# Kernel optimization log

Measured on AMD Instinct MI355X. Metric: run time of the kernel, lower is better.

The kernel has to match this reference:

```python
import jax, jax.numpy as jnp
import numpy as np

N_NODES = 100000
N_EDGES = 1600000
F_IN = 64
F_OUT = 64


def setup_inputs() -> dict:
    key = jax.random.key(0)
    k1, k2, k3 = jax.random.split(key, 3)
    x = jax.random.normal(k1, (1, 1, N_NODES, F_IN), dtype=jnp.float32)
    edge_index = jax.random.randint(k2, (2, N_EDGES), 0, N_NODES, dtype=jnp.int32)
    # xavier-init linear weight [F_IN, F_OUT], zero bias (xavier_zero_bias)
    scale = jnp.sqrt(2.0 / (F_IN + F_OUT)).astype(jnp.float32)
    weight = jax.random.normal(k3, (F_IN, F_OUT), dtype=jnp.float32) * scale
    bias = jnp.zeros((F_OUT,), dtype=jnp.float32)
    return {"x": x, "edge_index": edge_index, "weight": weight, "bias": bias}


def reference(x, edge_index, weight, bias):
    # x: [B, T, N, F_in]
    B, T, N, _ = x.shape
    # linear transform
    h = jnp.einsum('btnf,fo->btno', x, weight) + bias  # [B,T,N,F_out]
    # add self loops
    loops = jnp.arange(N, dtype=edge_index.dtype)
    src = jnp.concatenate([edge_index[0], loops])  # [E+N]
    dst = jnp.concatenate([edge_index[1], loops])  # [E+N]
    w = jnp.ones(src.shape[0], dtype=h.dtype)
    # symmetric GCN normalization: D^{-1/2} A D^{-1/2} (degree over dst)
    deg = jnp.zeros((N,), dtype=h.dtype).at[dst].add(w)
    inv_sqrt = jnp.clip(deg, 1e-9) ** -0.5
    norm = inv_sqrt[dst] * w * inv_sqrt[src]  # [E+N]
    # gather src features, scale by norm, scatter-add to dst
    msg = h[:, :, src, :] * norm[None, None, :, None]  # [B,T,E+N,F_out]
    out = jnp.zeros_like(h).at[:, :, dst, :].add(msg)  # [B,T,N,F_out]
    # GraphConvBase post: activation (gelu), dropout=0, norm=identity
    return jax.nn.gelu(out)
```

## Files before the change

### kernel.cpp

```cpp
#include <hip/hip_runtime.h>
#include <hip/hip_fp16.h>
#include <math.h>

#define N_NODES 100000
#define N_EDGES 1600000
#define F_DIM 64
#define BSH 9
#define BNODES 512
#define NBUCK ((N_NODES + BNODES - 1) / BNODES)
#define CAP 16384
#define EPT 8
#define TILE (256 * EPT)

__global__ __launch_bounds__(256) void init_k(int* __restrict__ bcur) {
    int i = blockIdx.x * 256 + threadIdx.x;
    if (i < NBUCK) bcur[i] = i * CAP;
}

__global__ __launch_bounds__(256) void pass1_k(const int* __restrict__ src,
                                               const int* __restrict__ dst,
                                               int* __restrict__ bcur,
                                               unsigned int* __restrict__ tmp, int E) {
    __shared__ int lcnt[NBUCK];
    __shared__ int lbase[NBUCK];
    for (int i = threadIdx.x; i < NBUCK; i += 256) lcnt[i] = 0;
    __syncthreads();

    int4 sreg[EPT / 4], dreg[EPT / 4];
    int base4 = blockIdx.x * (TILE / 4);
#pragma unroll
    for (int j = 0; j < EPT / 4; ++j) {
        int i4 = base4 + j * 256 + threadIdx.x;
        if (i4 < E / 4) {
            sreg[j] = ((const int4*)src)[i4];
            dreg[j] = ((const int4*)dst)[i4];
            atomicAdd(&lcnt[dreg[j].x >> BSH], 1);
            atomicAdd(&lcnt[dreg[j].y >> BSH], 1);
            atomicAdd(&lcnt[dreg[j].z >> BSH], 1);
            atomicAdd(&lcnt[dreg[j].w >> BSH], 1);
        } else {
            dreg[j].x = -1;
        }
    }
    __syncthreads();
    for (int b = threadIdx.x; b < NBUCK; b += 256) {
        int c = lcnt[b];
        lbase[b] = c ? atomicAdd(&bcur[b], c) : 0;
        lcnt[b] = 0;
    }
    __syncthreads();
#pragma unroll
    for (int j = 0; j < EPT / 4; ++j) {
        if (dreg[j].x >= 0) {
            int d, s, b, r;
            d = dreg[j].x; s = sreg[j].x; b = d >> BSH;
            r = atomicAdd(&lcnt[b], 1);
            tmp[lbase[b] + r] = (unsigned int)s | ((unsigned int)(d & (BNODES - 1)) << 17);
            d = dreg[j].y; s = sreg[j].y; b = d >> BSH;
            r = atomicAdd(&lcnt[b], 1);
            tmp[lbase[b] + r] = (unsigned int)s | ((unsigned int)(d & (BNODES - 1)) << 17);
            d = dreg[j].z; s = sreg[j].z; b = d >> BSH;
            r = atomicAdd(&lcnt[b], 1);
            tmp[lbase[b] + r] = (unsigned int)s | ((unsigned int)(d & (BNODES - 1)) << 17);
            d = dreg[j].w; s = sreg[j].w; b = d >> BSH;
            r = atomicAdd(&lcnt[b], 1);
            tmp[lbase[b] + r] = (unsigned int)s | ((unsigned int)(d & (BNODES - 1)) << 17);
        }
    }
}

__global__ __launch_bounds__(512) void passB_k(unsigned int* __restrict__ tmp,
                                               const int* __restrict__ bcur,
                                               unsigned int* __restrict__ rowinfo,
                                               float* __restrict__ inv) {
    __shared__ unsigned int buf[CAP];
    __shared__ int cnt[BNODES];
    __shared__ int cur[BNODES];
    __shared__ int ls[BNODES];
    int b = blockIdx.x;
    int beg0 = b * CAP;
    int cntb = bcur[b] - beg0;
    int tid = threadIdx.x;

    cnt[tid] = 0;
    __syncthreads();
    for (int i = tid; i < cntb; i += 512) {
        unsigned int v = tmp[beg0 + i];
        buf[i] = v;
        atomicAdd(&cnt[v >> 17], 1);
    }
    __syncthreads();

    int a = cnt[tid];
    ls[tid] = a;
    __syncthreads();
    for (int off = 1; off < BNODES; off <<= 1) {
        int p = (tid >= off) ? ls[tid - off] : 0;
        __syncthreads();
        ls[tid] += p;
        __syncthreads();
    }
    int p0 = beg0 + ls[tid] - a;
    cur[tid] = p0;
    int n = (b << BSH) + tid;
    if (n < N_NODES) {
        rowinfo[n] = (unsigned int)p0 | ((unsigned int)a << 22);
        inv[n] = rsqrtf((float)(a + 1));
    }
    __syncthreads();

    for (int i = tid; i < cntb; i += 512) {
        unsigned int v = buf[i];
        int pos = atomicAdd(&cur[v >> 17], 1);
        tmp[pos] = v & 0x1FFFFu;
    }
}

__global__ __launch_bounds__(128) void linear_k(const float* __restrict__ x,
                                                const float* __restrict__ W,
                                                const float* __restrict__ bias,
                                                const float* __restrict__ inv,
                                                __half* __restrict__ h, int N) {
    __shared__ float Ws[F_DIM][F_DIM];
    __shared__ float bs[F_DIM];
    for (int i = threadIdx.x; i < F_DIM * F_DIM; i += 128) Ws[i >> 6][i & 63] = W[i];
    if (threadIdx.x < F_DIM) bs[threadIdx.x] = bias[threadIdx.x];
    __syncthreads();

    int n = blockIdx.x * 128 + threadIdx.x;
    if (n >= N) return;

    float xr[F_DIM];
    const float4* xp = (const float4*)(x + (size_t)n * F_DIM);
#pragma unroll
    for (int k4 = 0; k4 < 16; ++k4) {
        float4 v = xp[k4];
        xr[k4 * 4 + 0] = v.x; xr[k4 * 4 + 1] = v.y;
        xr[k4 * 4 + 2] = v.z; xr[k4 * 4 + 3] = v.w;
    }
    float invn = inv[n];
    __half* hp = h + (size_t)n * F_DIM;
#pragma unroll 1
    for (int f0 = 0; f0 < F_DIM; f0 += 4) {
        float a0 = bs[f0 + 0], a1 = bs[f0 + 1], a2 = bs[f0 + 2], a3 = bs[f0 + 3];
#pragma unroll
        for (int k = 0; k < F_DIM; ++k) {
            float xv = xr[k];
            a0 += xv * Ws[k][f0 + 0];
            a1 += xv * Ws[k][f0 + 1];
            a2 += xv * Ws[k][f0 + 2];
            a3 += xv * Ws[k][f0 + 3];
        }
        union { __half2 h2[2]; float2 f2; } u;
        u.h2[0] = __floats2half2_rn(a0 * invn, a1 * invn);
        u.h2[1] = __floats2half2_rn(a2 * invn, a3 * invn);
        *((float2*)(hp + f0)) = u.f2;
    }
}

__device__ __forceinline__ float gelu1(float x) {
    float x3 = x * x * x;
    float t = tanhf(0.7978845608028654f * (x + 0.044715f * x3));
    return 0.5f * x * (1.0f + t);
}

__global__ __launch_bounds__(256) void gather_k(const __half* __restrict__ h,
                                                const float* __restrict__ inv,
                                                const unsigned int* __restrict__ rowinfo,
                                                const unsigned int* __restrict__ esrc,
                                                float* __restrict__ out, int N) {
    int n = blockIdx.x * 4 + (threadIdx.x >> 6);
    if (n >= N) return;
    int lane = threadIdx.x & 63;
    int eslot = lane >> 4;
    int fq = lane & 15;

    unsigned int ri = rowinfo[n];
    int beg = (int)(ri & 0x3FFFFFu);
    int deg = (int)(ri >> 22);

    __half2 acc0 = __floats2half2_rn(0.f, 0.f);
    __half2 acc1 = acc0;
    int k = eslot;
    for (; k + 12 < deg; k += 16) {
        int s0 = (int)esrc[beg + k];
        int s1 = (int)esrc[beg + k + 4];
        int s2 = (int)esrc[beg + k + 8];
        int s3 = (int)esrc[beg + k + 12];
        union { float2 f; __half2 h2[2]; } u0, u1, u2, u3;
        u0.f = *((const float2*)(h + (size_t)s0 * F_DIM) + fq);
        u1.f = *((const float2*)(h + (size_t)s1 * F_DIM) + fq);
        u2.f = *((const float2*)(h + (size_t)s2 * F_DIM) + fq);
        u3.f = *((const float2*)(h + (size_t)s3 * F_DIM) + fq);
        acc0 = __hadd2(acc0, __hadd2(__hadd2(u0.h2[0], u1.h2[0]), __hadd2(u2.h2[0], u3.h2[0])));
        acc1 = __hadd2(acc1, __hadd2(__hadd2(u0.h2[1], u1.h2[1]), __hadd2(u2.h2[1], u3.h2[1])));
    }
    for (; k < deg; k += 4) {
        int s0 = (int)esrc[beg + k];
        union { float2 f; __half2 h2[2]; } u0;
        u0.f = *((const float2*)(h + (size_t)s0 * F_DIM) + fq);
        acc0 = __hadd2(acc0, u0.h2[0]);
        acc1 = __hadd2(acc1, u0.h2[1]);
    }
    float2 a = __half22float2(acc0);
    float2 b2 = __half22float2(acc1);
    float ax = a.x, ay = a.y, az = b2.x, aw = b2.y;
    ax += __shfl_xor(ax, 16); ay += __shfl_xor(ay, 16);
    az += __shfl_xor(az, 16); aw += __shfl_xor(aw, 16);
    ax += __shfl_xor(ax, 32); ay += __shfl_xor(ay, 32);
    az += __shfl_xor(az, 32); aw += __shfl_xor(aw, 32);

    if (eslot == 0) {
        float invn = inv[n];
        union { float2 f; __half2 h2[2]; } us;
        us.f = *((const float2*)(h + (size_t)n * F_DIM) + fq);
        float2 s0 = __half22float2(us.h2[0]);
        float2 s1 = __half22float2(us.h2[1]);
        float4 o;
        o.x = gelu1((ax + s0.x) * invn);
        o.y = gelu1((ay + s0.y) * invn);
        o.z = gelu1((az + s1.x) * invn);
        o.w = gelu1((aw + s1.y) * invn);
        ((float4*)(out + (size_t)n * F_DIM))[fq] = o;
    }
}

extern "C" void kernel_launch(void* const* d_in, const int* in_sizes, int n_in,
                              void* d_out, int out_size, void* d_ws, size_t ws_size,
                              hipStream_t stream) {
    const float* x    = (const float*)d_in[0];
    const int*   ei   = (const int*)d_in[1];
    const float* W    = (const float*)d_in[2];
    const float* bias = (const float*)d_in[3];
    float* out = (float*)d_out;

    const int* src = ei;
    const int* dst = ei + N_EDGES;

    unsigned int* tmp     = (unsigned int*)d_ws;
    unsigned int* rowinfo = tmp + (size_t)NBUCK * CAP;
    float*        inv     = (float*)(rowinfo + N_NODES);
    int*          bcur    = (int*)(inv + N_NODES);
    size_t off = (size_t)(bcur + NBUCK) - (size_t)d_ws;
    off = (off + 31) & ~(size_t)31;
    __half* h = (__half*)((char*)d_ws + off);

    init_k<<<(NBUCK + 255) / 256, 256, 0, stream>>>(bcur);
    pass1_k<<<(N_EDGES + TILE - 1) / TILE, 256, 0, stream>>>(src, dst, bcur, tmp, N_EDGES);
    passB_k<<<NBUCK, 512, 0, stream>>>(tmp, bcur, rowinfo, inv);
    linear_k<<<(N_NODES + 127) / 128, 128, 0, stream>>>(x, W, bias, inv, h, N_NODES);
    gather_k<<<(N_NODES + 3) / 4, 256, 0, stream>>>(h, inv, rowinfo, tmp, out, N_NODES);
}
```

Measured before the change: 131.1 us.

## Fuse edge bucketing with linear transform and move source normalization into gather

Edge bucketing and the dense linear transform now run in one launch, with blocks split by index, so the two independent phases overlap. Because the linear stage no longer needs per-node degrees, the source-side inverse-sqrt scaling moves into the gather, which reads inv[src] per edge and accumulates in fp32 FMAs instead of fp16 adds. passB drops its shared staging buffer, writes into a separate esrc array with 1024 threads, and bucket counters are zeroed by a memset instead of an init kernel. EPT and CAP change as well. The cost is an extra random inv load per edge and more ALU work in the gather. CAP=12288 also leaves less headroom against bucket overflow.

```diff
diff --git a/kernel.cpp b/kernel.cpp
--- a/kernel.cpp
+++ b/kernel.cpp
@@ -8,153 +8,149 @@
 #define BSH 9
 #define BNODES 512
 #define NBUCK ((N_NODES + BNODES - 1) / BNODES)
-#define CAP 16384
-#define EPT 8
+#define CAP 12288
+#define EPT 32
 #define TILE (256 * EPT)
-
-__global__ __launch_bounds__(256) void init_k(int* __restrict__ bcur) {
-    int i = blockIdx.x * 256 + threadIdx.x;
-    if (i < NBUCK) bcur[i] = i * CAP;
-}
-
-__global__ __launch_bounds__(256) void pass1_k(const int* __restrict__ src,
-                                               const int* __restrict__ dst,
-                                               int* __restrict__ bcur,
-                                               unsigned int* __restrict__ tmp, int E) {
-    __shared__ int lcnt[NBUCK];
-    __shared__ int lbase[NBUCK];
-    for (int i = threadIdx.x; i < NBUCK; i += 256) lcnt[i] = 0;
-    __syncthreads();
-
-    int4 sreg[EPT / 4], dreg[EPT / 4];
-    int base4 = blockIdx.x * (TILE / 4);
-#pragma unroll
-    for (int j = 0; j < EPT / 4; ++j) {
-        int i4 = base4 + j * 256 + threadIdx.x;
-        if (i4 < E / 4) {
-            sreg[j] = ((const int4*)src)[i4];
-            dreg[j] = ((const int4*)dst)[i4];
-            atomicAdd(&lcnt[dreg[j].x >> BSH], 1);
-            atomicAdd(&lcnt[dreg[j].y >> BSH], 1);
-            atomicAdd(&lcnt[dreg[j].z >> BSH], 1);
-            atomicAdd(&lcnt[dreg[j].w >> BSH], 1);
-        } else {
-            dreg[j].x = -1;
-        }
-    }
-    __syncthreads();
-    for (int b = threadIdx.x; b < NBUCK; b += 256) {
-        int c = lcnt[b];
-        lbase[b] = c ? atomicAdd(&bcur[b], c) : 0;
-        lcnt[b] = 0;
-    }
-    __syncthreads();
-#pragma unroll
-    for (int j = 0; j < EPT / 4; ++j) {
-        if (dreg[j].x >= 0) {
-            int d, s, b, r;
-            d = dreg[j].x; s = sreg[j].x; b = d >> BSH;
-            r = atomicAdd(&lcnt[b], 1);
-            tmp[lbase[b] + r] = (unsigned int)s | ((unsigned int)(d & (BNODES - 1)) << 17);
-            d = dreg[j].y; s = sreg[j].y; b = d >> BSH;
-            r = atomicAdd(&lcnt[b], 1);
-            tmp[lbase[b] + r] = (unsigned int)s | ((unsigned int)(d & (BNODES - 1)) << 17);
-            d = dreg[j].z; s = sreg[j].z; b = d >> BSH;
-            r = atomicAdd(&lcnt[b], 1);
-            tmp[lbase[b] + r] = (unsigned int)s | ((unsigned int)(d & (BNODES - 1)) << 17);
-            d = dreg[j].w; s = sreg[j].w; b = d >> BSH;
-            r = atomicAdd(&lcnt[b], 1);
-            tmp[lbase[b] + r] = (unsigned int)s | ((unsigned int)(d & (BNODES - 1)) << 17);
-        }
-    }
-}
-
-__global__ __launch_bounds__(512) void passB_k(unsigned int* __restrict__ tmp,
-                                               const int* __restrict__ bcur,
-                                               unsigned int* __restrict__ rowinfo,
-                                               float* __restrict__ inv) {
-    __shared__ unsigned int buf[CAP];
+#define P1B ((N_EDGES + TILE - 1) / TILE)
+#define LINB ((N_NODES + 255) / 256)
+
+__global__ __launch_bounds__(256) void fused1_k(const int* __restrict__ src,
+                                                const int* __restrict__ dst,
+                                                int* __restrict__ bcur,
+                                                unsigned int* __restrict__ tmp,
+                                                const float* __restrict__ x,
+                                                const float* __restrict__ W,
+                                                const float* __restrict__ bias,
+                                                __half* __restrict__ h) {
+    if (blockIdx.x < P1B) {
+        __shared__ int lcnt[NBUCK];
+        __shared__ int lbase[NBUCK];
+        for (int i = threadIdx.x; i < NBUCK; i += 256) lcnt[i] = 0;
+        __syncthreads();
+
+        int4 sreg[EPT / 4], dreg[EPT / 4];
+        int base4 = blockIdx.x * (TILE / 4);
+#pragma unroll
+        for (int j = 0; j < EPT / 4; ++j) {
+            int i4 = base4 + j * 256 + threadIdx.x;
+            if (i4 < N_EDGES / 4) {
+                sreg[j] = ((const int4*)src)[i4];
+                dreg[j] = ((const int4*)dst)[i4];
+                atomicAdd(&lcnt[dreg[j].x >> BSH], 1);
+                atomicAdd(&lcnt[dreg[j].y >> BSH], 1);
+                atomicAdd(&lcnt[dreg[j].z >> BSH], 1);
+                atomicAdd(&lcnt[dreg[j].w >> BSH], 1);
+            } else {
+                dreg[j].x = -1;
+            }
+        }
+        __syncthreads();
+        for (int b = threadIdx.x; b < NBUCK; b += 256) {
+            int c = lcnt[b];
+            lbase[b] = c ? atomicAdd(&bcur[b], c) : 0;
+            lcnt[b] = 0;
+        }
+        __syncthreads();
+#pragma unroll
+        for (int j = 0; j < EPT / 4; ++j) {
+            if (dreg[j].x >= 0) {
+                int d, s, b, r;
+                d = dreg[j].x; s = sreg[j].x; b = d >> BSH;
+                r = atomicAdd(&lcnt[b], 1);
+                tmp[(size_t)b * CAP + lbase[b] + r] = (unsigned int)s | ((unsigned int)(d & (BNODES - 1)) << 17);
+                d = dreg[j].y; s = sreg[j].y; b = d >> BSH;
+                r = atomicAdd(&lcnt[b], 1);
+                tmp[(size_t)b * CAP + lbase[b] + r] = (unsigned int)s | ((unsigned int)(d & (BNODES - 1)) << 17);
+                d = dreg[j].z; s = sreg[j].z; b = d >> BSH;
+                r = atomicAdd(&lcnt[b], 1);
+                tmp[(size_t)b * CAP + lbase[b] + r] = (unsigned int)s | ((unsigned int)(d & (BNODES - 1)) << 17);
+                d = dreg[j].w; s = sreg[j].w; b = d >> BSH;
+                r = atomicAdd(&lcnt[b], 1);
+                tmp[(size_t)b * CAP + lbase[b] + r] = (unsigned int)s | ((unsigned int)(d & (BNODES - 1)) << 17);
+            }
+        }
+    } else {
+        __shared__ float Ws[F_DIM][F_DIM];
+        __shared__ float bs[F_DIM];
+        for (int i = threadIdx.x; i < F_DIM * F_DIM; i += 256) Ws[i >> 6][i & 63] = W[i];
+        if (threadIdx.x < F_DIM) bs[threadIdx.x] = bias[threadIdx.x];
+        __syncthreads();
+
+        int n = (blockIdx.x - P1B) * 256 + threadIdx.x;
+        if (n >= N_NODES) return;
+
+        float xr[F_DIM];
+        const float4* xp = (const float4*)(x + (size_t)n * F_DIM);
+#pragma unroll
+        for (int k4 = 0; k4 < 16; ++k4) {
+            float4 v = xp[k4];
+            xr[k4 * 4 + 0] = v.x; xr[k4 * 4 + 1] = v.y;
+            xr[k4 * 4 + 2] = v.z; xr[k4 * 4 + 3] = v.w;
+        }
+        __half* hp = h + (size_t)n * F_DIM;
+#pragma unroll 1
+        for (int f0 = 0; f0 < F_DIM; f0 += 4) {
+            float a0 = bs[f0 + 0], a1 = bs[f0 + 1], a2 = bs[f0 + 2], a3 = bs[f0 + 3];
+#pragma unroll
+            for (int k = 0; k < F_DIM; ++k) {
+                float xv = xr[k];
+                a0 += xv * Ws[k][f0 + 0];
+                a1 += xv * Ws[k][f0 + 1];
+                a2 += xv * Ws[k][f0 + 2];
+                a3 += xv * Ws[k][f0 + 3];
+            }
+            union { __half2 h2[2]; float2 f2; } u;
+            u.h2[0] = __floats2half2_rn(a0, a1);
+            u.h2[1] = __floats2half2_rn(a2, a3);
+            *((float2*)(hp + f0)) = u.f2;
+        }
+    }
+}
+
+__global__ __launch_bounds__(1024) void passB_k(const unsigned int* __restrict__ tmp,
+                                                const int* __restrict__ bcur,
+                                                unsigned int* __restrict__ esrc,
+                                                unsigned int* __restrict__ rowinfo,
+                                                float* __restrict__ inv) {
     __shared__ int cnt[BNODES];
     __shared__ int cur[BNODES];
     __shared__ int ls[BNODES];
     int b = blockIdx.x;
+    int tid = threadIdx.x;
     int beg0 = b * CAP;
-    int cntb = bcur[b] - beg0;
-    int tid = threadIdx.x;
-
-    cnt[tid] = 0;
-    __syncthreads();
-    for (int i = tid; i < cntb; i += 512) {
+    int cntb = bcur[b];
+
+    if (tid < BNODES) cnt[tid] = 0;
+    __syncthreads();
+    for (int i = tid; i < cntb; i += 1024)
+        atomicAdd(&cnt[tmp[beg0 + i] >> 17], 1);
+    __syncthreads();
+
+    int a = 0;
+    if (tid < BNODES) { a = cnt[tid]; ls[tid] = a; }
+    __syncthreads();
+    for (int off = 1; off < BNODES; off <<= 1) {
+        int p = 0;
+        if (tid < BNODES && tid >= off) p = ls[tid - off];
+        __syncthreads();
+        if (tid < BNODES) ls[tid] += p;
+        __syncthreads();
+    }
+    if (tid < BNODES) {
+        int p0 = beg0 + ls[tid] - a;
+        cur[tid] = p0;
+        int n = (b << BSH) + tid;
+        if (n < N_NODES) {
+            rowinfo[n] = (unsigned int)p0 | ((unsigned int)a << 22);
+            inv[n] = rsqrtf((float)(a + 1));
+        }
+    }
+    __syncthreads();
+
+    for (int i = tid; i < cntb; i += 1024) {
         unsigned int v = tmp[beg0 + i];
-        buf[i] = v;
-        atomicAdd(&cnt[v >> 17], 1);
-    }
-    __syncthreads();
-
-    int a = cnt[tid];
-    ls[tid] = a;
-    __syncthreads();
-    for (int off = 1; off < BNODES; off <<= 1) {
-        int p = (tid >= off) ? ls[tid - off] : 0;
-        __syncthreads();
-        ls[tid] += p;
-        __syncthreads();
-    }
-    int p0 = beg0 + ls[tid] - a;
-    cur[tid] = p0;
-    int n = (b << BSH) + tid;
-    if (n < N_NODES) {
-        rowinfo[n] = (unsigned int)p0 | ((unsigned int)a << 22);
-        inv[n] = rsqrtf((float)(a + 1));
-    }
-    __syncthreads();
-
-    for (int i = tid; i < cntb; i += 512) {
-        unsigned int v = buf[i];
         int pos = atomicAdd(&cur[v >> 17], 1);
-        tmp[pos] = v & 0x1FFFFu;
-    }
-}
-
-__global__ __launch_bounds__(128) void linear_k(const float* __restrict__ x,
-                                                const float* __restrict__ W,
-                                                const float* __restrict__ bias,
-                                                const float* __restrict__ inv,
-                                                __half* __restrict__ h, int N) {
-    __shared__ float Ws[F_DIM][F_DIM];
-    __shared__ float bs[F_DIM];
-    for (int i = threadIdx.x; i < F_DIM * F_DIM; i += 128) Ws[i >> 6][i & 63] = W[i];
-    if (threadIdx.x < F_DIM) bs[threadIdx.x] = bias[threadIdx.x];
-    __syncthreads();
-
-    int n = blockIdx.x * 128 + threadIdx.x;
-    if (n >= N) return;
-
-    float xr[F_DIM];
-    const float4* xp = (const float4*)(x + (size_t)n * F_DIM);
-#pragma unroll
-    for (int k4 = 0; k4 < 16; ++k4) {
-        float4 v = xp[k4];
-        xr[k4 * 4 + 0] = v.x; xr[k4 * 4 + 1] = v.y;
-        xr[k4 * 4 + 2] = v.z; xr[k4 * 4 + 3] = v.w;
-    }
-    float invn = inv[n];
-    __half* hp = h + (size_t)n * F_DIM;
-#pragma unroll 1
-    for (int f0 = 0; f0 < F_DIM; f0 += 4) {
-        float a0 = bs[f0 + 0], a1 = bs[f0 + 1], a2 = bs[f0 + 2], a3 = bs[f0 + 3];
-#pragma unroll
-        for (int k = 0; k < F_DIM; ++k) {
-            float xv = xr[k];
-            a0 += xv * Ws[k][f0 + 0];
-            a1 += xv * Ws[k][f0 + 1];
-            a2 += xv * Ws[k][f0 + 2];
-            a3 += xv * Ws[k][f0 + 3];
-        }
-        union { __half2 h2[2]; float2 f2; } u;
-        u.h2[0] = __floats2half2_rn(a0 * invn, a1 * invn);
-        u.h2[1] = __floats2half2_rn(a2 * invn, a3 * invn);
-        *((float2*)(hp + f0)) = u.f2;
+        esrc[pos] = v & 0x1FFFFu;
     }
 }
 
@@ -179,32 +175,38 @@
     int beg = (int)(ri & 0x3FFFFFu);
     int deg = (int)(ri >> 22);
 
-    __half2 acc0 = __floats2half2_rn(0.f, 0.f);
-    __half2 acc1 = acc0;
+    float ax = 0.f, ay = 0.f, az = 0.f, aw = 0.f;
     int k = eslot;
     for (; k + 12 < deg; k += 16) {
         int s0 = (int)esrc[beg + k];
         int s1 = (int)esrc[beg + k + 4];
         int s2 = (int)esrc[beg + k + 8];
         int s3 = (int)esrc[beg + k + 12];
+        float w0 = inv[s0], w1 = inv[s1], w2 = inv[s2], w3 = inv[s3];
         union { float2 f; __half2 h2[2]; } u0, u1, u2, u3;
         u0.f = *((const float2*)(h + (size_t)s0 * F_DIM) + fq);
         u1.f = *((const float2*)(h + (size_t)s1 * F_DIM) + fq);
         u2.f = *((const float2*)(h + (size_t)s2 * F_DIM) + fq);
         u3.f = *((const float2*)(h + (size_t)s3 * F_DIM) + fq);
-        acc0 = __hadd2(acc0, __hadd2(__hadd2(u0.h2[0], u1.h2[0]), __hadd2(u2.h2[0], u3.h2[0])));
-        acc1 = __hadd2(acc1, __hadd2(__hadd2(u0.h2[1], u1.h2[1]), __hadd2(u2.h2[1], u3.h2[1])));
+        float2 a, b;
+        a = __half22float2(u0.h2[0]); b = __half22float2(u0.h2[1]);
+        ax = fmaf(a.x, w0, ax); ay = fmaf(a.y, w0, ay); az = fmaf(b.x, w0, az); aw = fmaf(b.y, w0, aw);
+        a = __half22float2(u1.h2[0]); b = __half22float2(u1.h2[1]);
+        ax = fmaf(a.x, w1, ax); ay = fmaf(a.y, w1, ay); az = fmaf(b.x, w1, az); aw = fmaf(b.y, w1, aw);
+        a = __half22float2(u2.h2[0]); b = __half22float2(u2.h2[1]);
+        ax = fmaf(a.x, w2, ax); ay = fmaf(a.y, w2, ay); az = fmaf(b.x, w2, az); aw = fmaf(b.y, w2, aw);
+        a = __half22float2(u3.h2[0]); b = __half22float2(u3.h2[1]);
+        ax = fmaf(a.x, w3, ax); ay = fmaf(a.y, w3, ay); az = fmaf(b.x, w3, az); aw = fmaf(b.y, w3, aw);
     }
     for (; k < deg; k += 4) {
         int s0 = (int)esrc[beg + k];
+        float w0 = inv[s0];
         union { float2 f; __half2 h2[2]; } u0;
         u0.f = *((const float2*)(h + (size_t)s0 * F_DIM) + fq);
-        acc0 = __hadd2(acc0, u0.h2[0]);
-        acc1 = __hadd2(acc1, u0.h2[1]);
-    }
-    float2 a = __half22float2(acc0);
-    float2 b2 = __half22float2(acc1);
-    float ax = a.x, ay = a.y, az = b2.x, aw = b2.y;
+        float2 a = __half22float2(u0.h2[0]);
+        float2 b = __half22float2(u0.h2[1]);
+        ax = fmaf(a.x, w0, ax); ay = fmaf(a.y, w0, ay); az = fmaf(b.x, w0, az); aw = fmaf(b.y, w0, aw);
+    }
     ax += __shfl_xor(ax, 16); ay += __shfl_xor(ay, 16);
     az += __shfl_xor(az, 16); aw += __shfl_xor(aw, 16);
     ax += __shfl_xor(ax, 32); ay += __shfl_xor(ay, 32);
@@ -217,10 +219,10 @@
         float2 s0 = __half22float2(us.h2[0]);
         float2 s1 = __half22float2(us.h2[1]);
         float4 o;
-        o.x = gelu1((ax + s0.x) * invn);
-        o.y = gelu1((ay + s0.y) * invn);
-        o.z = gelu1((az + s1.x) * invn);
-        o.w = gelu1((aw + s1.y) * invn);
+        o.x = gelu1((ax + s0.x * invn) * invn);
+        o.y = gelu1((ay + s0.y * invn) * invn);
+        o.z = gelu1((az + s1.x * invn) * invn);
+        o.w = gelu1((aw + s1.y * invn) * invn);
         ((float4*)(out + (size_t)n * F_DIM))[fq] = o;
     }
 }
@@ -238,16 +240,17 @@
     const int* dst = ei + N_EDGES;
 
     unsigned int* tmp     = (unsigned int*)d_ws;
-    unsigned int* rowinfo = tmp + (size_t)NBUCK * CAP;
+    unsigned int* esrc    = tmp + (size_t)NBUCK * CAP;
+    unsigned int* rowinfo = esrc + (size_t)NBUCK * CAP;
     float*        inv     = (float*)(rowinfo + N_NODES);
     int*          bcur    = (int*)(inv + N_NODES);
     size_t off = (size_t)(bcur + NBUCK) - (size_t)d_ws;
     off = (off + 31) & ~(size_t)31;
     __half* h = (__half*)((char*)d_ws + off);
 
-    init_k<<<(NBUCK + 255) / 256, 256, 0, stream>>>(bcur);
-    pass1_k<<<(N_EDGES + TILE - 1) / TILE, 256, 0, stream>>>(src, dst, bcur, tmp, N_EDGES);
-    passB_k<<<NBUCK, 512, 0, stream>>>(tmp, bcur, rowinfo, inv);
-    linear_k<<<(N_NODES + 127) / 128, 128, 0, stream>>>(x, W, bias, inv, h, N_NODES);
-    gather_k<<<(N_NODES + 3) / 4, 256, 0, stream>>>(h, inv, rowinfo, tmp, out, N_NODES);
-}
+    hipMemsetAsync(bcur, 0, NBUCK * sizeof(int), stream);
+
+    fused1_k<<<P1B + LINB, 256, 0, stream>>>(src, dst, bcur, tmp, x, W, bias, h);
+    passB_k<<<NBUCK, 1024, 0, stream>>>(tmp, bcur, esrc, rowinfo, inv);
+    gather_k<<<(N_NODES + 3) / 4, 256, 0, stream>>>(h, inv, rowinfo, esrc, out, N_NODES);
+}
```

Result: faster. 113.8 us (median of 2 runs) (-13.2%).
